# Optimization experiments

Hardware: AMD Instinct MI355X
Metric: run time of the kernel (lower is better)

The kernel has to match this reference:

```python
import jax, jax.numpy as jnp
import numpy as np

B, H, S, D = 2, 12, 2048, 128
SCALE = D ** (-0.5)
LAMBDA_INIT = 0.8


def setup_inputs() -> dict:
    key = jax.random.key(0)
    ks = jax.random.split(key, 5)
    shp = (B, H, S, D)
    return {
        "q1": jax.random.normal(ks[0], shp, dtype=jnp.float32),
        "k1": jax.random.normal(ks[1], shp, dtype=jnp.float32),
        "v": jax.random.normal(ks[2], shp, dtype=jnp.float32),
        "q2": jax.random.normal(ks[3], shp, dtype=jnp.float32),
        "k2": jax.random.normal(ks[4], shp, dtype=jnp.float32),
        # learnable lambda parameter, stored in log space (lambda_init=0.8)
        "lambda_log": jnp.full((1,), np.log(LAMBDA_INIT), dtype=jnp.float32),
    }


def _causal_attn(q, k, v, causal_mask):
    # q,k,v: [B,H,S,D]; causal_mask: [S,S] bool (True = keep)
    scores = jnp.einsum("bhqd,bhkd->bhqk", q, k) * SCALE
    neg = jnp.asarray(jnp.finfo(scores.dtype).min, scores.dtype)
    scores = jnp.where(causal_mask, scores, neg)
    weights = jax.nn.softmax(scores, axis=-1)
    return jnp.einsum("bhqk,bhkd->bhqd", weights, v)


def reference(q1, k1, v, q2, k2, lambda_log):
    seq = q1.shape[2]
    causal_mask = jnp.tril(jnp.ones((seq, seq), dtype=bool))
    attn1 = _causal_attn(q1, k1, v, causal_mask)
    attn2 = _causal_attn(q2, k2, v, causal_mask)
    lambda_val = jnp.exp(lambda_log).astype(q1.dtype)  # scalar-shaped (1,)
    return attn1 - lambda_val * attn2
```

## Files before the change

kernel.cpp:

```cpp
#include <hip/hip_runtime.h>

#define S_LEN 2048
#define D_DIM 128
#define NBH   24
#define TELEM (NBH * S_LEN * D_DIM)
#define SC2  (0.08838834764831845f * 1.44269504088896f)
#define MFIX 20.0f

typedef __bf16 bf16x8 __attribute__((ext_vector_type(8)));
typedef float f32x4 __attribute__((ext_vector_type(4)));
union Frag { bf16x8 v; unsigned short h[8]; uint4 q; };

#define PSTR 40
#define BUFU 12288
#define SMEM_USH (2 * BUFU)

__device__ __forceinline__ unsigned short f2bf(float f) {
    union { float f; unsigned u; } x; x.f = f;
    unsigned r = x.u + 0x7fffu + ((x.u >> 16) & 1u);
    return (unsigned short)(r >> 16);
}
__device__ __forceinline__ unsigned pk2bf(float a, float b) {
    return (unsigned)f2bf(a) | ((unsigned)f2bf(b) << 16);
}
__device__ __forceinline__ float wred(float x) {
    x += __shfl_xor(x, 16);
    x += __shfl_xor(x, 32);
    return x;
}
__device__ __forceinline__ void butterfly(const float* p, Frag& pf) {
    unsigned a0 = pk2bf(p[0], p[1]);
    unsigned a1 = pk2bf(p[2], p[3]);
    unsigned a2 = pk2bf(p[4], p[5]);
    unsigned a3 = pk2bf(p[6], p[7]);
    asm("v_permlane32_swap_b32 %0, %1" : "+v"(a0), "+v"(a2));
    asm("v_permlane32_swap_b32 %0, %1" : "+v"(a1), "+v"(a3));
    asm("v_permlane16_swap_b32 %0, %1" : "+v"(a0), "+v"(a2));
    asm("v_permlane16_swap_b32 %0, %1" : "+v"(a1), "+v"(a3));
    pf.q = (uint4){a0, a1, a2, a3};
}

typedef __attribute__((address_space(1))) const unsigned int gu32;
typedef __attribute__((address_space(3))) unsigned int lu32;
__device__ __forceinline__ void g2l16(const unsigned short* g, unsigned short* l) {
    __builtin_amdgcn_global_load_lds((gu32*)g, (lu32*)l, 16, 0, 0);
}

#define KBLK (TELEM / (8 * 256))
__global__ __launch_bounds__(256) void conv_kv(
    const float* __restrict__ gk1, const float* __restrict__ gk2, const float* __restrict__ gv,
    unsigned short* __restrict__ ok1, unsigned short* __restrict__ ok2,
    unsigned short* __restrict__ ovt)
{
    __shared__ __align__(16) unsigned short sT[128 * 40];
    const int b = blockIdx.x;
    if (b < 2 * KBLK) {
        const float* src = (b < KBLK) ? gk1 : gk2;
        unsigned short* dst = (b < KBLK) ? ok1 : ok2;
        const int bb = (b < KBLK) ? b : b - KBLK;
        const size_t base = ((size_t)bb * 256 + threadIdx.x) * 8;
        float4 a = *(const float4*)(src + base);
        float4 c = *(const float4*)(src + base + 4);
        uint4 w = {pk2bf(a.x, a.y), pk2bf(a.z, a.w), pk2bf(c.x, c.y), pk2bf(c.z, c.w)};
        *(uint4*)(dst + base) = w;
        return;
    }
    const int bx  = b - 2 * KBLK;
    const int tid  = threadIdx.x;
    const int wave = tid >> 6;
    const int lane = tid & 63;
    const int quad = lane >> 4;
    const int l16  = lane & 15;
    const int bh = bx >> 6;
    const int s0 = (bx & 63) * 32;
    const float* pv = gv + (size_t)bh * S_LEN * D_DIM + (size_t)s0 * D_DIM;
    const int vd0 = (wave >> 1) * 64 + l16 * 4;
    const int pq  = ((quad & 1) << 1) | (quad >> 1);
    #pragma unroll
    for (int i = 0; i < 4; ++i) {
        const int kvb = i * 8 + (wave & 1) * 4;
        float4 f = *(const float4*)(pv + (kvb + quad) * D_DIM + vd0);
        unsigned h01 = pk2bf(f.x, f.y), h23 = pk2bf(f.z, f.w);
        unsigned t01 = (unsigned)__shfl_xor((int)h01, 16);
        unsigned t23 = (unsigned)__shfl_xor((int)h23, 16);
        unsigned b01, b23;
        if (quad & 1) {
            b01 = (t23 & 0xffffu) | (h23 << 16);
            b23 = (t23 >> 16) | (h23 & 0xffff0000u);
        } else {
            b01 = (h01 & 0xffffu) | (t01 << 16);
            b23 = (h01 >> 16) | (t01 & 0xffff0000u);
        }
        unsigned s01 = (unsigned)__shfl_xor((int)b01, 32);
        unsigned s23 = (unsigned)__shfl_xor((int)b23, 32);
        uint2 w;
        if (quad & 2) { w.x = s23; w.y = b23; }
        else          { w.x = b01; w.y = s01; }
        *(uint2*)&sT[(vd0 + pq) * 40 + kvb] = w;
    }
    __syncthreads();
    const int d = tid >> 1;
    const int h = tid & 1;
    uint4 w0 = *(const uint4*)&sT[d * 40 + h * 16];
    uint4 w1 = *(const uint4*)&sT[d * 40 + h * 16 + 8];
    unsigned short* out = ovt + ((size_t)bh * D_DIM + d) * S_LEN + s0 + h * 16;
    *(uint4*)(out) = w0;
    *(uint4*)(out + 8) = w1;
}

__device__ __forceinline__ void stage_tile(
    unsigned short* smem, int boff, int w,
    const int* koff, const int* voff,
    const unsigned short* k1pl, const unsigned short* k2pl, const unsigned short* vpl,
    int kv0)
{
    const unsigned short* kp1 = k1pl + (size_t)kv0 * 128;
    const unsigned short* kp2 = k2pl + (size_t)kv0 * 128;
    const unsigned short* vp  = vpl + kv0;
    unsigned short* dk1 = smem + boff + w * 1024;
    unsigned short* dk2 = smem + boff + 4096 + w * 1024;
    unsigned short* dv  = smem + boff + 8192 + w * 1024;
    #pragma unroll
    for (int j = 0; j < 2; ++j) {
        g2l16(kp1 + koff[j], dk1 + j * 512);
        g2l16(kp2 + koff[j], dk2 + j * 512);
        g2l16(vp  + voff[j], dv  + j * 512);
    }
}

__device__ __forceinline__ void half_body(
    int l16, int quad, int t, int qv2, bool full,
    const Frag (&qf)[4], f32x4 (&o)[8], float& la,
    const unsigned short* sK, const unsigned short* sVt)
{
    f32x4 s[2];
    s[0] = (f32x4){0.f, 0.f, 0.f, 0.f};
    s[1] = (f32x4){0.f, 0.f, 0.f, 0.f};
    __builtin_amdgcn_s_setprio(1);
    #pragma unroll
    for (int sub = 0; sub < 2; ++sub) {
        const int srow = (sub * 16 + l16) * 128;
        #pragma unroll
        for (int ks = 0; ks < 4; ++ks) {
            const int c = ks * 4 + quad;
            Frag kf;
            kf.q = *(const uint4*)&sK[srow + ((c ^ l16) << 3)];
            s[sub] = __builtin_amdgcn_mfma_f32_16x16x32_bf16(kf.v, qf[ks].v, s[sub], 0, 0, 0);
        }
    }
    __builtin_amdgcn_s_setprio(0);
    float p[8];
    if (full) {
        #pragma unroll
        for (int sub = 0; sub < 2; ++sub)
            #pragma unroll
            for (int r = 0; r < 4; ++r)
                p[sub * 4 + r] = __builtin_amdgcn_exp2f(s[sub][r] * SC2 - MFIX);
    } else {
        #pragma unroll
        for (int sub = 0; sub < 2; ++sub)
            #pragma unroll
            for (int r = 0; r < 4; ++r) {
                const int kv = t * 32 + sub * 16 + quad * 4 + r;
                p[sub * 4 + r] = __builtin_amdgcn_exp2f((kv <= qv2) ? s[sub][r] * SC2 - MFIX : -1e30f);
            }
    }
    float a = 0.f;
    #pragma unroll
    for (int i = 0; i < 8; ++i) a += p[i];
    la += a;
    Frag pf;
    butterfly(p, pf);
    __builtin_amdgcn_s_setprio(1);
    #pragma unroll
    for (int cb = 0; cb < 8; ++cb) {
        const int d = cb * 16 + l16;
        Frag vf;
        vf.q = *(const uint4*)&sVt[d * 32 + ((quad ^ ((d >> 1) & 3)) << 3)];
        o[cb] = __builtin_amdgcn_mfma_f32_16x16x32_bf16(vf.v, pf.v, o[cb], 0, 0, 0);
    }
    __builtin_amdgcn_s_setprio(0);
}

__global__ __launch_bounds__(256, 3) void diff_attn_fast(
    const float* __restrict__ gq1, const float* __restrict__ gq2,
    const float* __restrict__ gll,
    const unsigned short* __restrict__ k1b, const unsigned short* __restrict__ k2b,
    const unsigned short* __restrict__ vtb, float* __restrict__ gout)
{
    __shared__ __align__(16) unsigned short smem[SMEM_USH];

    const int tid  = threadIdx.x;
    const int w    = tid >> 6;
    const int lane = tid & 63;
    const int quad = lane >> 4;
    const int l16  = lane & 15;
    const int g    = w & 1;

    const int bid   = blockIdx.x;
    const int pairi = bid / NBH;
    const int bh    = bid - pairi * NBH;
    const int sAi   = 63 - pairi;
    const int T     = 64 - pairi;
    const int qw    = (w < 2) ? sAi * 32 : pairi * 32;
    const size_t hoff = (size_t)bh * (S_LEN * D_DIM);

    const float lam = __expf(gll[0]);

    Frag q1f[4], q2f[4];
    {
        const float* p1 = gq1 + hoff + (size_t)(qw + g * 16 + l16) * D_DIM;
        const float* p2 = gq2 + hoff + (size_t)(qw + g * 16 + l16) * D_DIM;
        #pragma unroll
        for (int ks = 0; ks < 4; ++ks) {
            const int d0 = ks * 32 + quad * 8;
            float4 a = *(const float4*)(p1 + d0);
            float4 b = *(const float4*)(p1 + d0 + 4);
            q1f[ks].q = (uint4){pk2bf(a.x, a.y), pk2bf(a.z, a.w),
                                pk2bf(b.x, b.y), pk2bf(b.z, b.w)};
            a = *(const float4*)(p2 + d0);
            b = *(const float4*)(p2 + d0 + 4);
            q2f[ks].q = (uint4){pk2bf(a.x, a.y), pk2bf(a.z, a.w),
                                pk2bf(b.x, b.y), pk2bf(b.z, b.w)};
        }
    }

    int koff[2], voff[2];
    #pragma unroll
    for (int jj = 0; jj < 2; ++jj) {
        const int s = w * 8 + jj * 4 + quad;
        koff[jj] = s * 128 + ((l16 ^ (s & 15)) << 3);
        const int d = w * 32 + jj * 16 + (lane >> 2);
        voff[jj] = d * 2048 + (((lane & 3) ^ ((d >> 1) & 3)) << 3);
    }
    const unsigned short* k1pl = k1b + hoff;
    const unsigned short* k2pl = k2b + hoff;
    const unsigned short* vpl  = vtb + hoff;

    f32x4 o1[8], o2[8];
    #pragma unroll
    for (int ii = 0; ii < 8; ++ii) {
        o1[ii] = (f32x4){0.f, 0.f, 0.f, 0.f};
        o2[ii] = (f32x4){0.f, 0.f, 0.f, 0.f};
    }
    float l1a = 0.f, l2a = 0.f;

    __asm__ __volatile__("s_waitcnt vmcnt(0)" ::: "memory");
    stage_tile(smem, 0, w, koff, voff, k1pl, k2pl, vpl, 0);

    int boff = 0;
    const int qv = qw + g * 16 + l16;
    for (int t = 0; t <= pairi; ++t) {
        __asm__ __volatile__("s_waitcnt vmcnt(0) lgkmcnt(0)" ::: "memory");
        __builtin_amdgcn_s_barrier();
        __asm__ __volatile__("" ::: "memory");
        if (t + 1 < T)
            stage_tile(smem, boff ^ BUFU, w, koff, voff, k1pl, k2pl, vpl, (t + 1) * 32);

        const unsigned short* sK1 = smem + boff;
        const unsigned short* sK2 = smem + boff + 4096;
        const unsigned short* sVt = smem + boff + 8192;
        const int kv0 = t * 32;

        f32x4 sA[2], sB[2];
        #pragma unroll
        for (int sub = 0; sub < 2; ++sub) {
            sA[sub] = (f32x4){0.f, 0.f, 0.f, 0.f};
            sB[sub] = (f32x4){0.f, 0.f, 0.f, 0.f};
        }
        __builtin_amdgcn_s_setprio(1);
        #pragma unroll
        for (int sub = 0; sub < 2; ++sub) {
            const int srow = (sub * 16 + l16) * 128;
            #pragma unroll
            for (int ks = 0; ks < 4; ++ks) {
                const int c = ks * 4 + quad;
                Frag kf;
                kf.q = *(const uint4*)&sK1[srow + ((c ^ l16) << 3)];
                sA[sub] = __builtin_amdgcn_mfma_f32_16x16x32_bf16(kf.v, q1f[ks].v, sA[sub], 0, 0, 0);
                kf.q = *(const uint4*)&sK2[srow + ((c ^ l16) << 3)];
                sB[sub] = __builtin_amdgcn_mfma_f32_16x16x32_bf16(kf.v, q2f[ks].v, sB[sub], 0, 0, 0);
            }
        }
        __builtin_amdgcn_s_setprio(0);

        const bool full = (w < 2) || (t < pairi);
        float p1v[8], p2v[8];
        if (full) {
            #pragma unroll
            for (int sub = 0; sub < 2; ++sub)
                #pragma unroll
                for (int r = 0; r < 4; ++r) {
                    p1v[sub * 4 + r] = __builtin_amdgcn_exp2f(sA[sub][r] * SC2 - MFIX);
                    p2v[sub * 4 + r] = __builtin_amdgcn_exp2f(sB[sub][r] * SC2 - MFIX);
                }
        } else {
            #pragma unroll
            for (int sub = 0; sub < 2; ++sub)
                #pragma unroll
                for (int r = 0; r < 4; ++r) {
                    const int kv = kv0 + sub * 16 + quad * 4 + r;
                    const bool ok = (kv <= qv);
                    p1v[sub * 4 + r] = __builtin_amdgcn_exp2f(ok ? sA[sub][r] * SC2 - MFIX : -1e30f);
                    p2v[sub * 4 + r] = __builtin_amdgcn_exp2f(ok ? sB[sub][r] * SC2 - MFIX : -1e30f);
                }
        }
        float a1 = 0.f, a2 = 0.f;
        #pragma unroll
        for (int ii = 0; ii < 8; ++ii) { a1 += p1v[ii]; a2 += p2v[ii]; }
        l1a += a1; l2a += a2;

        Frag pf1, pf2;
        butterfly(p1v, pf1);
        butterfly(p2v, pf2);

        __builtin_amdgcn_s_setprio(1);
        #pragma unroll
        for (int cb = 0; cb < 8; ++cb) {
            const int d = cb * 16 + l16;
            Frag vf;
            vf.q = *(const uint4*)&sVt[d * 32 + ((quad ^ ((d >> 1) & 3)) << 3)];
            o1[cb] = __builtin_amdgcn_mfma_f32_16x16x32_bf16(vf.v, pf1.v, o1[cb], 0, 0, 0);
            o2[cb] = __builtin_amdgcn_mfma_f32_16x16x32_bf16(vf.v, pf2.v, o2[cb], 0, 0, 0);
        }
        __builtin_amdgcn_s_setprio(0);
        boff ^= BUFU;
    }

    if (w >= 2) {
        const float l1 = wred(l1a);
        const float l2 = wred(l2a);
        const float inv1 = 1.0f / l1;
        const float inv2 = lam / l2;
        float* outp = gout + hoff + (size_t)(qw + g * 16 + l16) * D_DIM + quad * 4;
        #pragma unroll
        for (int cb = 0; cb < 8; ++cb) {
            f32x4 r = o1[cb] * inv1 - o2[cb] * inv2;
            *(f32x4*)(outp + cb * 16) = r;
        }
        const float* p2 = gq2 + hoff + (size_t)(sAi * 32 + g * 16 + l16) * D_DIM;
        #pragma unroll
        for (int ks = 0; ks < 4; ++ks) {
            const int d0 = ks * 32 + quad * 8;
            float4 a = *(const float4*)(p2 + d0);
            float4 b = *(const float4*)(p2 + d0 + 4);
            q2f[ks].q = (uint4){pk2bf(a.x, a.y), pk2bf(a.z, a.w),
                                pk2bf(b.x, b.y), pk2bf(b.z, b.w)};
        }
        #pragma unroll
        for (int ii = 0; ii < 8; ++ii) o2[ii] = (f32x4){0.f, 0.f, 0.f, 0.f};
        l2a = 0.f;
    }

    const int qv2 = sAi * 32 + g * 16 + l16;
    for (int t = pairi + 1; t < T; ++t) {
        __asm__ __volatile__("s_waitcnt vmcnt(0) lgkmcnt(0)" ::: "memory");
        __builtin_amdgcn_s_barrier();
        __asm__ __volatile__("" ::: "memory");
        if (t + 1 < T)
            stage_tile(smem, boff ^ BUFU, w, koff, voff, k1pl, k2pl, vpl, (t + 1) * 32);

        const unsigned short* sVt = smem + boff + 8192;
        const bool full = (t < sAi);
        if (w < 2)
            half_body(l16, quad, t, qv2, full, q1f, o1, l1a, smem + boff, sVt);
        else
            half_body(l16, quad, t, qv2, full, q2f, o2, l2a, smem + boff + 4096, sVt);
        boff ^= BUFU;
    }

    __asm__ __volatile__("s_waitcnt lgkmcnt(0)" ::: "memory");
    __builtin_amdgcn_s_barrier();
    __asm__ __volatile__("" ::: "memory");
    if (w >= 2) {
        float* dst = (float*)smem + g * 2368;
        const int base = lane * 37;
        #pragma unroll
        for (int cb = 0; cb < 8; ++cb)
            *(f32x4*)&dst[base + cb * 4] = o2[cb];
        dst[base + 32] = l2a;
    }
    __asm__ __volatile__("s_waitcnt lgkmcnt(0)" ::: "memory");
    __builtin_amdgcn_s_barrier();
    __asm__ __volatile__("" ::: "memory");
    if (w < 2) {
        const float* src = (const float*)smem + g * 2368;
        const int base = lane * 37;
        #pragma unroll
        for (int cb = 0; cb < 8; ++cb)
            o2[cb] += *(const f32x4*)&src[base + cb * 4];
        l2a += src[base + 32];
        const float l1 = wred(l1a);
        const float l2 = wred(l2a);
        const float inv1 = 1.0f / l1;
        const float inv2 = lam / l2;
        float* outp = gout + hoff + (size_t)(qw + g * 16 + l16) * D_DIM + quad * 4;
        #pragma unroll
        for (int cb = 0; cb < 8; ++cb) {
            f32x4 r = o1[cb] * inv1 - o2[cb] * inv2;
            *(f32x4*)(outp + cb * 16) = r;
        }
    }
}

#define KSTR 136
#define VSTR2 40
#define foK1 0
#define foK2 (32 * KSTR)
#define foVt (2 * 32 * KSTR)
#define foP  (2 * 32 * KSTR + 128 * VSTR2)
#define FSMEM (foP + 4 * 2 * 16 * PSTR)

__global__ __launch_bounds__(256) void diff_attn_slow(
    const float* __restrict__ gq1, const float* __restrict__ gk1,
    const float* __restrict__ gv,  const float* __restrict__ gq2,
    const float* __restrict__ gk2, const float* __restrict__ gll,
    float* __restrict__ gout)
{
    __shared__ __align__(16) unsigned short smem[FSMEM];
    unsigned short* sK1 = smem + foK1;
    unsigned short* sK2 = smem + foK2;
    unsigned short* sVt = smem + foVt;

    const int tid  = threadIdx.x;
    const int wave = tid >> 6;
    const int lane = tid & 63;
    const int quad = lane >> 4;
    const int l16  = lane & 15;
    const int qb   = (int)gridDim.x - 1 - (int)blockIdx.x;
    const int bh   = blockIdx.y;
    const size_t hoff = (size_t)bh * S_LEN * D_DIM;
    const int qbase = qb * 64 + wave * 16;

    unsigned short* sP1 = smem + foP + (wave * 2 + 0) * 16 * PSTR;
    unsigned short* sP2 = smem + foP + (wave * 2 + 1) * 16 * PSTR;

    const float lam = __expf(gll[0]);

    Frag q1f[4], q2f[4];
    {
        const float* p1 = gq1 + hoff + (size_t)(qbase + l16) * D_DIM;
        const float* p2 = gq2 + hoff + (size_t)(qbase + l16) * D_DIM;
        #pragma unroll
        for (int ks = 0; ks < 4; ++ks) {
            const int d0 = ks * 32 + quad * 8;
            float4 a = *(const float4*)(p1 + d0);
            float4 b = *(const float4*)(p1 + d0 + 4);
            q1f[ks].q = (uint4){pk2bf(a.x, a.y), pk2bf(a.z, a.w),
                               pk2bf(b.x, b.y), pk2bf(b.z, b.w)};
            a = *(const float4*)(p2 + d0);
            b = *(const float4*)(p2 + d0 + 4);
            q2f[ks].q = (uint4){pk2bf(a.x, a.y), pk2bf(a.z, a.w),
                               pk2bf(b.x, b.y), pk2bf(b.z, b.w)};
        }
    }

    f32x4 o1[8], o2[8];
    #pragma unroll
    for (int i = 0; i < 8; ++i) {
        o1[i] = (f32x4){0.f, 0.f, 0.f, 0.f};
        o2[i] = (f32x4){0.f, 0.f, 0.f, 0.f};
    }
    float m1 = -1e30f, m2 = -1e30f, l1 = 0.f, l2 = 0.f;

    const int ntiles  = qb * 2 + 2;
    const int mytiles = (qbase + 15) / 32 + 1;

    const int vd0 = (wave >> 1) * 64 + l16 * 4;
    const int pq  = ((quad & 1) << 1) | (quad >> 1);

    for (int t = 0; t < ntiles; ++t) {
        __syncthreads();
        const int kv0 = t * 32;
        {
            const float* pk1 = gk1 + hoff + (size_t)kv0 * D_DIM;
            const float* pk2 = gk2 + hoff + (size_t)kv0 * D_DIM;
            #pragma unroll
            for (int i = 0; i < 4; ++i) {
                const int e   = i * 256 + tid;
                const int row = e >> 5;
                const int c4  = e & 31;
                const int go  = row * D_DIM + c4 * 4;
                float4 f = *(const float4*)(pk1 + go);
                uint2 w; w.x = pk2bf(f.x, f.y); w.y = pk2bf(f.z, f.w);
                *(uint2*)&sK1[row * KSTR + c4 * 4] = w;
                f = *(const float4*)(pk2 + go);
                w.x = pk2bf(f.x, f.y); w.y = pk2bf(f.z, f.w);
                *(uint2*)&sK2[row * KSTR + c4 * 4] = w;
            }
        }
        {
            const float* pv = gv + hoff + (size_t)kv0 * D_DIM;
            #pragma unroll
            for (int i = 0; i < 4; ++i) {
                const int kvb = i * 8 + (wave & 1) * 4;
                float4 f = *(const float4*)(pv + (kvb + quad) * D_DIM + vd0);
                unsigned h01 = pk2bf(f.x, f.y), h23 = pk2bf(f.z, f.w);
                unsigned t01 = (unsigned)__shfl_xor((int)h01, 16);
                unsigned t23 = (unsigned)__shfl_xor((int)h23, 16);
                unsigned b01, b23;
                if (quad & 1) {
                    b01 = (t23 & 0xffffu) | (h23 << 16);
                    b23 = (t23 >> 16) | (h23 & 0xffff0000u);
                } else {
                    b01 = (h01 & 0xffffu) | (t01 << 16);
                    b23 = (h01 >> 16) | (t01 & 0xffff0000u);
                }
                unsigned s01 = (unsigned)__shfl_xor((int)b01, 32);
                unsigned s23 = (unsigned)__shfl_xor((int)b23, 32);
                uint2 w;
                if (quad & 2) { w.x = s23; w.y = b23; }
                else          { w.x = b01; w.y = s01; }
                *(uint2*)&sVt[(vd0 + pq) * VSTR2 + kvb] = w;
            }
        }
        __syncthreads();
        if (t >= mytiles) continue;

        f32x4 s1[2], s2[2];
        #pragma unroll
        for (int sub = 0; sub < 2; ++sub) {
            s1[sub] = (f32x4){0.f, 0.f, 0.f, 0.f};
            s2[sub] = (f32x4){0.f, 0.f, 0.f, 0.f};
            const int ro = (sub * 16 + l16) * KSTR + quad * 8;
            #pragma unroll
            for (int ks = 0; ks < 4; ++ks) {
                Frag kf;
                kf.q = *(const uint4*)&sK1[ro + ks * 32];
                s1[sub] = __builtin_amdgcn_mfma_f32_16x16x32_bf16(kf.v, q1f[ks].v, s1[sub], 0, 0, 0);
                kf.q = *(const uint4*)&sK2[ro + ks * 32];
                s2[sub] = __builtin_amdgcn_mfma_f32_16x16x32_bf16(kf.v, q2f[ks].v, s2[sub], 0, 0, 0);
            }
        }

        const int qv = qbase + l16;
        {
            float a[8];
            #pragma unroll
            for (int sub = 0; sub < 2; ++sub)
                #pragma unroll
                for (int r = 0; r < 4; ++r) {
                    const int kv = kv0 + sub * 16 + quad * 4 + r;
                    a[sub * 4 + r] = (kv <= qv) ? s1[sub][r] * SC2 : -__builtin_inff();
                }
            float mt = a[0];
            #pragma unroll
            for (int i = 1; i < 8; ++i) mt = fmaxf(mt, a[i]);
            mt = fmaxf(mt, __shfl_xor(mt, 16));
            mt = fmaxf(mt, __shfl_xor(mt, 32));
            const float mn = fmaxf(m1, mt);
            const float al = __builtin_amdgcn_exp2f(m1 - mn);
            m1 = mn;
            float p[8], rs = 0.f;
            #pragma unroll
            for (int i = 0; i < 8; ++i) { p[i] = __builtin_amdgcn_exp2f(a[i] - mn); rs += p[i]; }
            rs += __shfl_xor(rs, 16);
            rs += __shfl_xor(rs, 32);
            l1 = l1 * al + rs;
            #pragma unroll
            for (int cb = 0; cb < 8; ++cb) o1[cb] *= al;
            uint2 w;
            w.x = pk2bf(p[0], p[1]); w.y = pk2bf(p[2], p[3]);
            *(uint2*)&sP1[l16 * PSTR + quad * 4] = w;
            w.x = pk2bf(p[4], p[5]); w.y = pk2bf(p[6], p[7]);
            *(uint2*)&sP1[l16 * PSTR + 16 + quad * 4] = w;
        }
        {
            float a[8];
            #pragma unroll
            for (int sub = 0; sub < 2; ++sub)
                #pragma unroll
                for (int r = 0; r < 4; ++r) {
                    const int kv = kv0 + sub * 16 + quad * 4 + r;
                    a[sub * 4 + r] = (kv <= qv) ? s2[sub][r] * SC2 : -__builtin_inff();
                }
            float mt = a[0];
            #pragma unroll
            for (int i = 1; i < 8; ++i) mt = fmaxf(mt, a[i]);
            mt = fmaxf(mt, __shfl_xor(mt, 16));
            mt = fmaxf(mt, __shfl_xor(mt, 32));
            const float mn = fmaxf(m2, mt);
            const float al = __builtin_amdgcn_exp2f(m2 - mn);
            m2 = mn;
            float p[8], rs = 0.f;
            #pragma unroll
            for (int i = 0; i < 8; ++i) { p[i] = __builtin_amdgcn_exp2f(a[i] - mn); rs += p[i]; }
            rs += __shfl_xor(rs, 16);
            rs += __shfl_xor(rs, 32);
            l2 = l2 * al + rs;
            #pragma unroll
            for (int cb = 0; cb < 8; ++cb) o2[cb] *= al;
            uint2 w;
            w.x = pk2bf(p[0], p[1]); w.y = pk2bf(p[2], p[3]);
            *(uint2*)&sP2[l16 * PSTR + quad * 4] = w;
            w.x = pk2bf(p[4], p[5]); w.y = pk2bf(p[6], p[7]);
            *(uint2*)&sP2[l16 * PSTR + 16 + quad * 4] = w;
        }

        __asm__ __volatile__("s_waitcnt lgkmcnt(0)" ::: "memory");

        Frag pf1, pf2;
        pf1.q = *(const uint4*)&sP1[l16 * PSTR + quad * 8];
        pf2.q = *(const uint4*)&sP2[l16 * PSTR + quad * 8];
        #pragma unroll
        for (int cb = 0; cb < 8; ++cb) {
            Frag vf;
            vf.q = *(const uint4*)&sVt[(cb * 16 + l16) * VSTR2 + quad * 8];
            o1[cb] = __builtin_amdgcn_mfma_f32_16x16x32_bf16(vf.v, pf1.v, o1[cb], 0, 0, 0);
            o2[cb] = __builtin_amdgcn_mfma_f32_16x16x32_bf16(vf.v, pf2.v, o2[cb], 0, 0, 0);
        }
    }

    __syncthreads();
    float* sO = (float*)smem + wave * (16 * 132);
    const float inv1 = 1.0f / l1;
    const float inv2 = lam / l2;
    #pragma unroll
    for (int cb = 0; cb < 8; ++cb) {
        f32x4 r = o1[cb] * inv1 - o2[cb] * inv2;
        *(f32x4*)&sO[l16 * 132 + cb * 16 + quad * 4] = r;
    }
    __asm__ __volatile__("s_waitcnt lgkmcnt(0)" ::: "memory");
    #pragma unroll
    for (int u = 0; u < 8; ++u) {
        const int row = u * 2 + (lane >> 5);
        const int d4  = lane & 31;
        f32x4 vv = *(const f32x4*)&sO[row * 132 + d4 * 4];
        *(f32x4*)(gout + hoff + (size_t)(qbase + row) * D_DIM + d4 * 4) = vv;
    }
}

extern "C" void kernel_launch(void* const* d_in, const int* in_sizes, int n_in,
                              void* d_out, int out_size, void* d_ws, size_t ws_size,
                              hipStream_t stream) {
    (void)in_sizes; (void)n_in; (void)out_size;
    const float* gq1 = (const float*)d_in[0];
    const float* gk1 = (const float*)d_in[1];
    const float* gv  = (const float*)d_in[2];
    const float* gq2 = (const float*)d_in[3];
    const float* gk2 = (const float*)d_in[4];
    const float* gll = (const float*)d_in[5];
    float* gout = (float*)d_out;

    const size_t need = (size_t)3 * TELEM * sizeof(unsigned short);
    if (ws_size >= need) {
        unsigned short* k1b = (unsigned short*)d_ws;
        unsigned short* k2b = k1b + TELEM;
        unsigned short* vtb = k2b + TELEM;
        hipLaunchKernelGGL(conv_kv, dim3(2 * KBLK + NBH * (S_LEN / 32)), dim3(256), 0, stream,
                           gk1, gk2, gv, k1b, k2b, vtb);
        hipLaunchKernelGGL(diff_attn_fast, dim3(32 * NBH), dim3(256), 0, stream,
                           gq1, gq2, gll, k1b, k2b, vtb, gout);
    } else {
        hipLaunchKernelGGL(diff_attn_slow, dim3(S_LEN / 64, NBH), dim3(256), 0, stream,
                           gq1, gk1, gv, gq2, gk2, gll, gout);
    }
}
```

Before: 231.6 us.

## Load V fragments directly from global into registers, shrink LDS, raise occupancy

```diff
diff --git a/kernel.cpp b/kernel.cpp
--- a/kernel.cpp
+++ b/kernel.cpp
@@ -12,7 +12,7 @@
 union Frag { bf16x8 v; unsigned short h[8]; uint4 q; };
 
 #define PSTR 40
-#define BUFU 12288
+#define BUFU 8192
 #define SMEM_USH (2 * BUFU)
 
 __device__ __forceinline__ unsigned short f2bf(float f) {
@@ -109,29 +109,32 @@
 }
 
 __device__ __forceinline__ void stage_tile(
-    unsigned short* smem, int boff, int w,
-    const int* koff, const int* voff,
-    const unsigned short* k1pl, const unsigned short* k2pl, const unsigned short* vpl,
-    int kv0)
+    unsigned short* smem, int boff, int w, const int* koff,
+    const unsigned short* k1pl, const unsigned short* k2pl, int kv0)
 {
     const unsigned short* kp1 = k1pl + (size_t)kv0 * 128;
     const unsigned short* kp2 = k2pl + (size_t)kv0 * 128;
-    const unsigned short* vp  = vpl + kv0;
     unsigned short* dk1 = smem + boff + w * 1024;
     unsigned short* dk2 = smem + boff + 4096 + w * 1024;
-    unsigned short* dv  = smem + boff + 8192 + w * 1024;
     #pragma unroll
     for (int j = 0; j < 2; ++j) {
         g2l16(kp1 + koff[j], dk1 + j * 512);
         g2l16(kp2 + koff[j], dk2 + j * 512);
-        g2l16(vp  + voff[j], dv  + j * 512);
-    }
+    }
+}
+
+__device__ __forceinline__ void load_vfrags(
+    const unsigned short* vbase, int kv0, Frag (&vf)[8])
+{
+    #pragma unroll
+    for (int cb = 0; cb < 8; ++cb)
+        vf[cb].q = *(const uint4*)(vbase + cb * (16 * 2048) + kv0);
 }
 
 __device__ __forceinline__ void half_body(
     int l16, int quad, int t, int qv2, bool full,
-    const Frag (&qf)[4], f32x4 (&o)[8], float& la,
-    const unsigned short* sK, const unsigned short* sVt)
+    const Frag (&qf)[4], const Frag (&vf)[8], f32x4 (&o)[8], float& la,
+    const unsigned short* sK)
 {
     f32x4 s[2];
     s[0] = (f32x4){0.f, 0.f, 0.f, 0.f};
@@ -173,16 +176,12 @@
     butterfly(p, pf);
     __builtin_amdgcn_s_setprio(1);
     #pragma unroll
-    for (int cb = 0; cb < 8; ++cb) {
-        const int d = cb * 16 + l16;
-        Frag vf;
-        vf.q = *(const uint4*)&sVt[d * 32 + ((quad ^ ((d >> 1) & 3)) << 3)];
-        o[cb] = __builtin_amdgcn_mfma_f32_16x16x32_bf16(vf.v, pf.v, o[cb], 0, 0, 0);
-    }
+    for (int cb = 0; cb < 8; ++cb)
+        o[cb] = __builtin_amdgcn_mfma_f32_16x16x32_bf16(vf[cb].v, pf.v, o[cb], 0, 0, 0);
     __builtin_amdgcn_s_setprio(0);
 }
 
-__global__ __launch_bounds__(256, 3) void diff_attn_fast(
+__global__ __launch_bounds__(256, 4) void diff_attn_fast(
     const float* __restrict__ gq1, const float* __restrict__ gq2,
     const float* __restrict__ gll,
     const unsigned short* __restrict__ k1b, const unsigned short* __restrict__ k2b,
@@ -225,17 +224,15 @@
         }
     }
 
-    int koff[2], voff[2];
+    int koff[2];
     #pragma unroll
     for (int jj = 0; jj < 2; ++jj) {
         const int s = w * 8 + jj * 4 + quad;
         koff[jj] = s * 128 + ((l16 ^ (s & 15)) << 3);
-        const int d = w * 32 + jj * 16 + (lane >> 2);
-        voff[jj] = d * 2048 + (((lane & 3) ^ ((d >> 1) & 3)) << 3);
     }
     const unsigned short* k1pl = k1b + hoff;
     const unsigned short* k2pl = k2b + hoff;
-    const unsigned short* vpl  = vtb + hoff;
+    const unsigned short* vbase = vtb + (size_t)bh * (D_DIM * S_LEN) + l16 * 2048 + quad * 8;
 
     f32x4 o1[8], o2[8];
     #pragma unroll
@@ -246,7 +243,7 @@
     float l1a = 0.f, l2a = 0.f;
 
     __asm__ __volatile__("s_waitcnt vmcnt(0)" ::: "memory");
-    stage_tile(smem, 0, w, koff, voff, k1pl, k2pl, vpl, 0);
+    stage_tile(smem, 0, w, koff, k1pl, k2pl, 0);
 
     int boff = 0;
     const int qv = qw + g * 16 + l16;
@@ -254,13 +251,14 @@
         __asm__ __volatile__("s_waitcnt vmcnt(0) lgkmcnt(0)" ::: "memory");
         __builtin_amdgcn_s_barrier();
         __asm__ __volatile__("" ::: "memory");
+        const int kv0 = t * 32;
+        Frag vf[8];
+        load_vfrags(vbase, kv0, vf);
         if (t + 1 < T)
-            stage_tile(smem, boff ^ BUFU, w, koff, voff, k1pl, k2pl, vpl, (t + 1) * 32);
+            stage_tile(smem, boff ^ BUFU, w, koff, k1pl, k2pl, (t + 1) * 32);
 
         const unsigned short* sK1 = smem + boff;
         const unsigned short* sK2 = smem + boff + 4096;
-        const unsigned short* sVt = smem + boff + 8192;
-        const int kv0 = t * 32;
 
         f32x4 sA[2], sB[2];
         #pragma unroll
@@ -317,11 +315,8 @@
         __builtin_amdgcn_s_setprio(1);
         #pragma unroll
         for (int cb = 0; cb < 8; ++cb) {
-            const int d = cb * 16 + l16;
-            Frag vf;
-            vf.q = *(const uint4*)&sVt[d * 32 + ((quad ^ ((d >> 1) & 3)) << 3)];
-            o1[cb] = __builtin_amdgcn_mfma_f32_16x16x32_bf16(vf.v, pf1.v, o1[cb], 0, 0, 0);
-            o2[cb] = __builtin_amdgcn_mfma_f32_16x16x32_bf16(vf.v, pf2.v, o2[cb], 0, 0, 0);
+            o1[cb] = __builtin_amdgcn_mfma_f32_16x16x32_bf16(vf[cb].v, pf1.v, o1[cb], 0, 0, 0);
+            o2[cb] = __builtin_amdgcn_mfma_f32_16x16x32_bf16(vf[cb].v, pf2.v, o2[cb], 0, 0, 0);
         }
         __builtin_amdgcn_s_setprio(0);
         boff ^= BUFU;
@@ -357,15 +352,17 @@
         __asm__ __volatile__("s_waitcnt vmcnt(0) lgkmcnt(0)" ::: "memory");
         __builtin_amdgcn_s_barrier();
         __asm__ __volatile__("" ::: "memory");
+        const int kv0 = t * 32;
+        Frag vf[8];
+        load_vfrags(vbase, kv0, vf);
         if (t + 1 < T)
-            stage_tile(smem, boff ^ BUFU, w, koff, voff, k1pl, k2pl, vpl, (t + 1) * 32);
-
-        const unsigned short* sVt = smem + boff + 8192;
+            stage_tile(smem, boff ^ BUFU, w, koff, k1pl, k2pl, (t + 1) * 32);
+
         const bool full = (t < sAi);
         if (w < 2)
-            half_body(l16, quad, t, qv2, full, q1f, o1, l1a, smem + boff, sVt);
+            half_body(l16, quad, t, qv2, full, q1f, vf, o1, l1a, smem + boff);
         else
-            half_body(l16, quad, t, qv2, full, q2f, o2, l2a, smem + boff + 4096, sVt);
+            half_body(l16, quad, t, qv2, full, q2f, vf, o2, l2a, smem + boff + 4096);
         boff ^= BUFU;
     }
 
```

Measured after the change: 572.3 us. 2.47x slower.
